# Optimization experiments

Measured on AMD Instinct MI355X. Metric: run time of the kernel, lower is better.

## Reference

```python
import jax, jax.numpy as jnp
import numpy as np

B, D, H, W_ = 2, 256, 64, 64


def setup_inputs() -> dict:
    key = jax.random.key(0)
    k1, k2 = jax.random.split(key)
    x = jax.random.normal(k1, (B, D, H, W_), dtype=jnp.float32)
    W = jax.random.normal(k2, (3 * D, D), dtype=jnp.float32) * 0.02  # 1x1 conv weight [out,in]
    b = jnp.zeros((3 * D,), dtype=jnp.float32)
    return {"x": x, "W": W, "b": b}


def reference(x, W, b):
    Bs, d, h, w = x.shape
    N = h * w
    sqrtV = d ** 0.25  # sqrt(sqrt(d)); q,k each divided -> qk^T / sqrt(d)
    # 1x1 conv == per-pixel linear over channels
    qkv = jnp.einsum('bchw,oc->bohw', x, W) + b[None, :, None, None]
    q, k, v = jnp.split(qkv, 3, axis=1)
    q = q.reshape(Bs, d, N).transpose(0, 2, 1) / sqrtV  # [B,N,d]
    k = k.reshape(Bs, d, N).transpose(0, 2, 1) / sqrtV
    v = v.reshape(Bs, d, N).transpose(0, 2, 1)
    # Sinkhorn (eps=1, max_iter=1, uniform marginals 1/N), log domain.
    # cost C = -q k^T  =>  -C = q k^T (softmax-style logits)
    negC = jnp.einsum('bnd,bmd->bnm', q, k)  # [B,N,N]
    logm = jnp.log(1.0 / N + 1e-8).astype(x.dtype)
    u = logm - jax.nn.logsumexp(negC, axis=-1)            # [B,N] row update
    vpot = logm - jax.nn.logsumexp(negC + u[..., None], axis=-2)  # [B,N] col update
    pi = jnp.exp(negC + u[..., None] + vpot[:, None, :])  # transport plan = attn
    out = jnp.einsum('bnm,bmd->bnd', pi, v)               # [B,N,d]
    return out.transpose(0, 2, 1).reshape(Bs, d, h, w)
```

## Files before the change

kernel.cpp:

```cpp
#include <hip/hip_runtime.h>
#include <hip/hip_bf16.h>
#include <math.h>

typedef __bf16 bf16;
typedef __bf16 bf16x8 __attribute__((ext_vector_type(8)));
typedef __bf16 bf16x4 __attribute__((ext_vector_type(4)));
typedef float floatx4 __attribute__((ext_vector_type(4)));

typedef const __attribute__((address_space(1))) void* gas_t;
typedef __attribute__((address_space(3))) void* las_t;

#define NPIX 4096
#define DCH 256

#define OFF_XB   ((size_t)0)
#define OFF_WB   ((size_t)4194304)
#define OFF_Q    ((size_t)4587520)
#define OFF_K    ((size_t)8781824)
#define OFF_V    ((size_t)12976128)
#define OFF_E    ((size_t)17170432)
#define OFF_VPP  ((size_t)84279296)
#define OFF_RP   ((size_t)88473600)
#define OFF_CP   ((size_t)89522176)
#define OFF_PART ((size_t)90570752)

__device__ __forceinline__ void stage_tile(const bf16* __restrict__ g0, size_t rstride,
                                           bf16* lds, int t) {
  const int wbase = (t >> 6) << 6;
#pragma unroll
  for (int i = 0; i < 4; i++) {
    int slot = i * 256 + t;
    int row = slot >> 3, seg = slot & 7;
    const bf16* g = g0 + (size_t)row * rstride + ((seg ^ (row & 7)) << 3);
    bf16* l = lds + (size_t)(i * 256 + wbase) * 8;
    __builtin_amdgcn_global_load_lds((gas_t)g, (las_t)l, 16, 0, 0);
  }
}

__device__ __forceinline__ void stage_tile512(const bf16* __restrict__ g0, size_t rstride,
                                              bf16* lds, int t) {
  const int wbase = (t >> 6) << 6;
#pragma unroll
  for (int i = 0; i < 4; i++) {
    int slot = i * 512 + t;
    int row = slot >> 3, seg = slot & 7;
    const bf16* g = g0 + (size_t)row * rstride + ((seg ^ (row & 7)) << 3);
    bf16* l = lds + (size_t)(i * 512 + wbase) * 8;
    __builtin_amdgcn_global_load_lds((gas_t)g, (las_t)l, 16, 0, 0);
  }
}

__device__ __forceinline__ void stage_tile128_512(const bf16* __restrict__ g0, size_t rstride,
                                                  bf16* lds, int t) {
  const int wbase = (t >> 6) << 6;
#pragma unroll
  for (int i = 0; i < 2; i++) {
    int slot = i * 512 + t;
    int row = slot >> 3, seg = slot & 7;
    const bf16* g = g0 + (size_t)row * rstride + ((seg ^ (row & 7)) << 3);
    bf16* l = lds + (size_t)(i * 512 + wbase) * 8;
    __builtin_amdgcn_global_load_lds((gas_t)g, (las_t)l, 16, 0, 0);
  }
}

__global__ __launch_bounds__(256) void prep(
    const float* __restrict__ x, const float* __restrict__ W,
    bf16* __restrict__ xb, bf16* __restrict__ wb)
{
  const int t = threadIdx.x;
  if (blockIdx.y == 4) {
    int gid = (blockIdx.z * 64 + blockIdx.x) * 256 + t;
    for (int i = gid; i < 49152; i += 32768) {
      float4 v = *(const float4*)(W + (size_t)i * 4);
      bf16x4 pk = { (bf16)v.x, (bf16)v.y, (bf16)v.z, (bf16)v.w };
      *(bf16x4*)(wb + (size_t)i * 4) = pk;
    }
    return;
  }
  __shared__ float ts[64][65];
  const int b = blockIdx.z, n0 = blockIdx.x * 64, c0 = blockIdx.y * 64;
  const float* xp = x + ((size_t)b * DCH + c0) * NPIX + n0;
  for (int i = 0; i < 4; i++) {
    int slot = t + i * 256;
    int c = slot >> 4, nq = (slot & 15) * 4;
    float4 v = *(const float4*)(xp + (size_t)c * NPIX + nq);
    ts[c][nq + 0] = v.x; ts[c][nq + 1] = v.y; ts[c][nq + 2] = v.z; ts[c][nq + 3] = v.w;
  }
  __syncthreads();
  for (int i = 0; i < 2; i++) {
    int slot = t + i * 256;
    int n = slot >> 3, cq = (slot & 7) * 8;
    bf16x8 pk;
    for (int j = 0; j < 8; j++) pk[j] = (bf16)ts[cq + j][n];
    *(bf16x8*)(xb + ((size_t)b * NPIX + n0 + n) * DCH + c0 + cq) = pk;
  }
}

__global__ __launch_bounds__(256) void conv_mfma(
    const bf16* __restrict__ xb, const bf16* __restrict__ wb,
    const float* __restrict__ bias,
    bf16* __restrict__ qb, bf16* __restrict__ kb, bf16* __restrict__ vb)
{
  __shared__ bf16 at[2][128 * 64];
  __shared__ bf16 bt[2][128 * 64];
  __shared__ float bs[128];
  const int t  = threadIdx.x;
  const int n0 = blockIdx.x * 128;
  const int o0 = blockIdx.y * 128;
  if (t < 128) bs[t] = bias[o0 + t];
  const int lane = t & 63, wave = t >> 6;
  const int wm = wave >> 1, wn = wave & 1;
  const int l15 = lane & 15, quad = lane >> 4;
  const int l7 = l15 & 7;

  stage_tile(wb + (size_t)o0 * DCH, DCH, at[0], t);
  stage_tile(xb + (size_t)n0 * DCH, DCH, bt[0], t);

  floatx4 acc[4][4];
  for (int i=0;i<4;i++) for (int j=0;j<4;j++) for (int r=0;r<4;r++) acc[i][j][r] = 0.f;

#pragma unroll
  for (int kidx = 0; kidx < 4; kidx++) {
    const int cur = kidx & 1;
    if (kidx < 3) {
      stage_tile(wb + (size_t)o0 * DCH + (kidx + 1) * 64, DCH, at[cur ^ 1], t);
      stage_tile(xb + (size_t)n0 * DCH + (kidx + 1) * 64, DCH, bt[cur ^ 1], t);
      asm volatile("s_waitcnt vmcnt(8)" ::: "memory");
    } else {
      asm volatile("s_waitcnt vmcnt(0)" ::: "memory");
    }
    __builtin_amdgcn_s_barrier();
    asm volatile("" ::: "memory");
    for (int kk = 0; kk < 2; kk++) {
      bf16x8 af[4], bfr[4];
      int sw = ((kk * 4 + quad) ^ l7) * 8;
      for (int f = 0; f < 4; f++)
        af[f]  = *(const bf16x8*)&at[cur][(wm*64 + f*16 + l15)*64 + sw];
      for (int f = 0; f < 4; f++)
        bfr[f] = *(const bf16x8*)&bt[cur][(wn*64 + f*16 + l15)*64 + sw];
      for (int fm = 0; fm < 4; fm++)
        for (int fn = 0; fn < 4; fn++)
          acc[fm][fn] = __builtin_amdgcn_mfma_f32_16x16x32_bf16(af[fm], bfr[fn], acc[fm][fn], 0, 0, 0);
    }
    asm volatile("" ::: "memory");
    __builtin_amdgcn_s_barrier();
  }

  const float scale = (o0 < 512) ? 0.25f : 1.0f;
  bf16* dst; int od;
  if (o0 < 256)      { dst = qb; od = o0; }
  else if (o0 < 512) { dst = kb; od = o0 - 256; }
  else               { dst = vb; od = o0 - 512; }

  for (int fm = 0; fm < 4; fm++)
    for (int fn = 0; fn < 4; fn++) {
      int o_l = wm*64 + fm*16 + quad*4;
      int n_g = n0 + wn*64 + fn*16 + l15;
      bf16x4 pk;
      for (int r = 0; r < 4; r++)
        pk[r] = (bf16)((acc[fm][fn][r] + bs[o_l + r]) * scale);
      *(bf16x4*)(dst + (size_t)n_g * DCH + od + o_l) = pk;
    }
}

__global__ __launch_bounds__(512, 2) void pass_a(
    const bf16* __restrict__ qb, const bf16* __restrict__ kb,
    bf16* __restrict__ E, float* __restrict__ rowpartG)
{
  __shared__ bf16 smem[65536];
  int flat = (int)blockIdx.x + ((int)blockIdx.y << 4) + ((int)blockIdx.z << 8);
  flat = (flat & 7) * 64 + (flat >> 3);
  const int bx = flat & 15, by = (flat >> 4) & 15, b = flat >> 8;
  qb += (size_t)b * NPIX * DCH;
  kb += (size_t)b * NPIX * DCH;
  E  += (size_t)b * NPIX * NPIX;
  float* rp = rowpartG + ((size_t)b * 16 + bx) * NPIX;
  const int t  = threadIdx.x;
  const int m0 = bx * 256;
  const int n0 = by * 256;
  const int lane = t & 63, wave = t >> 6;
  const int wm = wave >> 2, wn = wave & 3;
  const int l15 = lane & 15, quad = lane >> 4;
  const int l7 = l15 & 7;
  bf16* kt0 = smem;
  bf16* qt0 = smem + 32768;

  stage_tile512(kb + (size_t)m0 * DCH, DCH, kt0, t);
  stage_tile512(qb + (size_t)n0 * DCH, DCH, qt0, t);

  floatx4 acc[8][4];
  for (int i=0;i<8;i++) for (int j=0;j<4;j++) for (int r=0;r<4;r++) acc[i][j][r] = 0.f;

#pragma unroll
  for (int kidx = 0; kidx < 4; kidx++) {
    const int cur = kidx & 1;
    if (kidx < 3) {
      stage_tile512(kb + (size_t)m0 * DCH + (kidx + 1) * 64, DCH, kt0 + (cur ^ 1) * 16384, t);
      stage_tile512(qb + (size_t)n0 * DCH + (kidx + 1) * 64, DCH, qt0 + (cur ^ 1) * 16384, t);
      asm volatile("s_waitcnt vmcnt(8)" ::: "memory");
    } else {
      asm volatile("s_waitcnt vmcnt(0)" ::: "memory");
    }
    __builtin_amdgcn_s_barrier();
    asm volatile("" ::: "memory");
    for (int kk = 0; kk < 2; kk++) {
      bf16x8 af[8], bfr[4];
      int sw = ((kk * 4 + quad) ^ l7) * 8;
      for (int f = 0; f < 8; f++)
        af[f]  = *(const bf16x8*)&kt0[cur*16384 + (wm*128 + f*16 + l15)*64 + sw];
      for (int f = 0; f < 4; f++)
        bfr[f] = *(const bf16x8*)&qt0[cur*16384 + (wn*64 + f*16 + l15)*64 + sw];
      for (int fm = 0; fm < 8; fm++)
        for (int fn = 0; fn < 4; fn++)
          acc[fm][fn] = __builtin_amdgcn_mfma_f32_16x16x32_bf16(af[fm], bfr[fn], acc[fm][fn], 0, 0, 0);
    }
    asm volatile("" ::: "memory");
    __builtin_amdgcn_s_barrier();
  }

  bf16* ep = smem;
  for (int fm = 0; fm < 8; fm++)
    for (int fn = 0; fn < 4; fn++) {
      int n_loc = wn*64 + fn*16 + l15;
      int mby  = (wm*128 + fm*16 + quad*4) * 2;
      int addr = n_loc * 512 + mby;
      addr ^= (n_loc & 7) << 4;
      bf16x4 pk;
      for (int r = 0; r < 4; r++) pk[r] = (bf16)__expf(acc[fm][fn][r]);
      *(bf16x4*)((char*)ep + addr) = pk;
    }
  __syncthreads();
#pragma unroll
  for (int i = 0; i < 16; i++) {
    int slot = i * 512 + t;
    int nr = slot >> 5, c = slot & 31;
    int addr = nr * 512 + c * 16;
    addr ^= (nr & 7) << 4;
    bf16x8 v = *(const bf16x8*)((char*)ep + addr);
    *(bf16x8*)(E + (size_t)(n0 + nr) * NPIX + m0 + c * 8) = v;
    float s = 0.f;
    for (int j = 0; j < 8; j++) s += (float)v[j];
    s += __shfl_xor(s, 1); s += __shfl_xor(s, 2); s += __shfl_xor(s, 4);
    s += __shfl_xor(s, 8); s += __shfl_xor(s, 16);
    if ((t & 31) == 0) rp[n0 + nr] = s;
  }
}

__global__ __launch_bounds__(256) void col_pass(
    const bf16* __restrict__ E, const float* __restrict__ rowpartG,
    float* __restrict__ colpartG, float logm)
{
  __shared__ float eus[128];
  const int b = blockIdx.z;
  E += (size_t)b * NPIX * NPIX;
  const float* rp = rowpartG + (size_t)b * 16 * NPIX;
  float* cp = colpartG + ((size_t)b * 32 + blockIdx.y) * NPIX;
  const int t = threadIdx.x;
  const int col = blockIdx.x * 1024 + t * 4;
  const int nbase = blockIdx.y * 128;
  if (t < 128) {
    float s = 0.f;
    for (int mi = 0; mi < 16; mi++) s += rp[(size_t)mi * NPIX + nbase + t];
    eus[t] = __expf(logm - __logf(s));
  }
  __syncthreads();
  float a0 = 0.f, a1 = 0.f, a2 = 0.f, a3 = 0.f;
  for (int r = 0; r < 128; r++) {
    float eu = eus[r];
    bf16x4 ev = *(const bf16x4*)(E + (size_t)(nbase + r) * NPIX + col);
    a0 += eu * (float)ev[0];
    a1 += eu * (float)ev[1];
    a2 += eu * (float)ev[2];
    a3 += eu * (float)ev[3];
  }
  float4 o = {a0, a1, a2, a3};
  *(float4*)(cp + col) = o;
}

__global__ __launch_bounds__(256) void vpp_kernel(
    const bf16* __restrict__ vb, const float* __restrict__ colpartG,
    bf16* __restrict__ vppT, float logm)
{
  __shared__ float ts[64][65];
  __shared__ float ef[64];
  const int b = blockIdx.z;
  vb += (size_t)b * NPIX * DCH;
  const float* cp = colpartG + (size_t)b * 32 * NPIX;
  vppT += (size_t)b * DCH * NPIX;
  const int t = threadIdx.x;
  const int m0 = blockIdx.x * 64, d0 = blockIdx.y * 64;
  if (t < 64) {
    float s = 0.f;
    for (int g = 0; g < 32; g++) s += cp[(size_t)g * NPIX + m0 + t];
    ef[t] = __expf(logm - __logf(s));
  }
  __syncthreads();
  for (int i = 0; i < 2; i++) {
    int slot = t + i * 256;
    int m = slot >> 3, dq = (slot & 7) * 8;
    bf16x8 v = *(const bf16x8*)(vb + (size_t)(m0 + m) * DCH + d0 + dq);
    float s = ef[m];
    for (int j = 0; j < 8; j++) ts[dq + j][m] = s * (float)v[j];
  }
  __syncthreads();
  for (int i = 0; i < 2; i++) {
    int slot = t + i * 256;
    int d = slot >> 3, mq = (slot & 7) * 8;
    bf16x8 pk;
    for (int j = 0; j < 8; j++) pk[j] = (bf16)ts[d][mq + j];
    *(bf16x8*)(vppT + (size_t)(d0 + d) * NPIX + m0 + mq) = pk;
  }
}

__global__ __launch_bounds__(512, 2) void pass_c(
    const bf16* __restrict__ E, const bf16* __restrict__ vppT,
    const float* __restrict__ rowpartG, bf16* __restrict__ part, float logm)
{
  __shared__ bf16 smem[49152];
  __shared__ float eus[128];
  const int z = blockIdx.z;
  const int b = z >> 2, kc = z & 3;
  E += (size_t)b * NPIX * NPIX;
  vppT += (size_t)b * DCH * NPIX;
  const float* rpg = rowpartG + (size_t)b * 16 * NPIX;
  part += (size_t)(b * 4 + kc) * DCH * NPIX;
  const int t  = threadIdx.x;
  const int n0 = blockIdx.x * 128;
  const int mstart = kc * 1024;
  if (t < 128) {
    float s = 0.f;
    for (int mi = 0; mi < 16; mi++) s += rpg[(size_t)mi * NPIX + n0 + t];
    eus[t] = __expf(logm - __logf(s));
  }
  const int lane = t & 63, wave = t >> 6;
  const int wn = wave >> 2, wd = wave & 3;
  const int l15 = lane & 15, quad = lane >> 4;
  const int l7 = l15 & 7;
  bf16* et0 = smem;
  bf16* vt0 = smem + 16384;

  floatx4 acc[4][4];
  for (int i=0;i<4;i++) for (int j=0;j<4;j++) for (int r=0;r<4;r++) acc[i][j][r] = 0.f;
  __syncthreads();

  stage_tile128_512(E + (size_t)n0 * NPIX + mstart, NPIX, et0, t);
  stage_tile512(vppT + mstart, NPIX, vt0, t);

#pragma unroll 4
  for (int kidx = 0; kidx < 16; kidx++) {
    const int cur = kidx & 1;
    if (kidx < 15) {
      const int kn = mstart + (kidx + 1) * 64;
      stage_tile128_512(E + (size_t)n0 * NPIX + kn, NPIX, et0 + (cur ^ 1) * 8192, t);
      stage_tile512(vppT + kn, NPIX, vt0 + (cur ^ 1) * 16384, t);
      asm volatile("s_waitcnt vmcnt(6)" ::: "memory");
    } else {
      asm volatile("s_waitcnt vmcnt(0)" ::: "memory");
    }
    __builtin_amdgcn_s_barrier();
    asm volatile("" ::: "memory");
    for (int kk = 0; kk < 2; kk++) {
      bf16x8 af[4], bfr[4];
      int sw = ((kk * 4 + quad) ^ l7) * 8;
      for (int f = 0; f < 4; f++)
        af[f]  = *(const bf16x8*)&et0[cur*8192  + (wn*64 + f*16 + l15)*64 + sw];
      for (int f = 0; f < 4; f++)
        bfr[f] = *(const bf16x8*)&vt0[cur*16384 + (wd*64 + f*16 + l15)*64 + sw];
      for (int fn = 0; fn < 4; fn++)
        for (int fd = 0; fd < 4; fd++)
          acc[fn][fd] = __builtin_amdgcn_mfma_f32_16x16x32_bf16(af[fn], bfr[fd], acc[fn][fd], 0, 0, 0);
    }
    asm volatile("" ::: "memory");
    __builtin_amdgcn_s_barrier();
  }

  bf16* ept = smem;
  for (int fn = 0; fn < 4; fn++)
    for (int fd = 0; fd < 4; fd++) {
      int d_loc = wd*64 + fd*16 + l15;
      int n_l   = wn*64 + fn*16 + quad*4;
      int addr = d_loc * 256 + n_l * 2;
      addr ^= (d_loc & 7) << 4;
      bf16x4 o;
      for (int r = 0; r < 4; r++) o[r] = (bf16)(acc[fn][fd][r] * eus[n_l + r]);
      *(bf16x4*)((char*)ept + addr) = o;
    }
  __syncthreads();
#pragma unroll
  for (int i = 0; i < 8; i++) {
    int slot = i * 512 + t;
    int dr = slot >> 4, c = slot & 15;
    int addr = dr * 256 + c * 16;
    addr ^= (dr & 7) << 4;
    bf16x8 v = *(const bf16x8*)((char*)ept + addr);
    *(bf16x8*)(part + (size_t)dr * NPIX + n0 + c * 8) = v;
  }
}

__global__ __launch_bounds__(256) void reduce_k(
    const bf16* __restrict__ part, float* __restrict__ outp)
{
  size_t i4 = ((size_t)blockIdx.x * 256 + threadIdx.x) * 4;
  size_t b = i4 >> 20;
  size_t off = i4 & (size_t)1048575;
  const bf16* p = part + b * 4 * (size_t)1048576 + off;
  bf16x4 a = *(const bf16x4*)(p);
  bf16x4 bq = *(const bf16x4*)(p + (size_t)1048576);
  bf16x4 c = *(const bf16x4*)(p + (size_t)2097152);
  bf16x4 d = *(const bf16x4*)(p + (size_t)3145728);
  float4 s = { (float)a[0]+(float)bq[0]+(float)c[0]+(float)d[0],
               (float)a[1]+(float)bq[1]+(float)c[1]+(float)d[1],
               (float)a[2]+(float)bq[2]+(float)c[2]+(float)d[2],
               (float)a[3]+(float)bq[3]+(float)c[3]+(float)d[3] };
  *(float4*)(outp + i4) = s;
}

extern "C" void kernel_launch(void* const* d_in, const int* in_sizes, int n_in,
                              void* d_out, int out_size, void* d_ws, size_t ws_size,
                              hipStream_t stream) {
  (void)in_sizes; (void)n_in; (void)out_size; (void)ws_size;
  const float* x    = (const float*)d_in[0];
  const float* Wm   = (const float*)d_in[1];
  const float* bias = (const float*)d_in[2];
  float* outp = (float*)d_out;
  char* ws = (char*)d_ws;

  bf16*  xb   = (bf16*)(ws + OFF_XB);
  bf16*  wb   = (bf16*)(ws + OFF_WB);
  bf16*  qb   = (bf16*)(ws + OFF_Q);
  bf16*  kb   = (bf16*)(ws + OFF_K);
  bf16*  vb   = (bf16*)(ws + OFF_V);
  bf16*  E    = (bf16*)(ws + OFF_E);
  bf16*  vppT = (bf16*)(ws + OFF_VPP);
  float* rp   = (float*)(ws + OFF_RP);
  float* cp   = (float*)(ws + OFF_CP);
  bf16*  part = (bf16*)(ws + OFF_PART);

  const float logm = logf(1.0f / 4096.0f + 1e-8f);

  prep<<<dim3(64, 5, 2), 256, 0, stream>>>(x, Wm, xb, wb);
  conv_mfma<<<dim3(64, 6), 256, 0, stream>>>(xb, wb, bias, qb, kb, vb);

  pass_a<<<dim3(16, 16, 2), 512, 0, stream>>>(qb, kb, E, rp);
  col_pass<<<dim3(4, 32, 2), 256, 0, stream>>>(E, rp, cp, logm);
  vpp_kernel<<<dim3(64, 4, 2), 256, 0, stream>>>(vb, cp, vppT, logm);
  pass_c<<<dim3(32, 1, 8), 512, 0, stream>>>(E, vppT, rp, part, logm);
  reduce_k<<<2048, 256, 0, stream>>>(part, outp);
}
```

Baseline: 152.6 us.

## Retile pass_c to 256-row tiles with 8-way split-K and XCD-aware block remap

pass_c now computes a 256(n)x256(d) output tile per block instead of 128x256, doubling A-fragment reuse of each staged vppT tile. The K range is split 8 ways instead of 4, keeping the grid at 256 blocks, and a flat block-index remap groups blocks across XCDs. reduce_k is extended to sum 8 bf16 partials, and col_pass's inner loop gets an unroll pragma. In exchange, partial-sum traffic doubles, and LDS use grows to about 128KB, which likely limits occupancy to one block per CU despite the launch bound.

```diff
diff --git a/kernel.cpp b/kernel.cpp
--- a/kernel.cpp
+++ b/kernel.cpp
@@ -42,19 +42,6 @@
   const int wbase = (t >> 6) << 6;
 #pragma unroll
   for (int i = 0; i < 4; i++) {
-    int slot = i * 512 + t;
-    int row = slot >> 3, seg = slot & 7;
-    const bf16* g = g0 + (size_t)row * rstride + ((seg ^ (row & 7)) << 3);
-    bf16* l = lds + (size_t)(i * 512 + wbase) * 8;
-    __builtin_amdgcn_global_load_lds((gas_t)g, (las_t)l, 16, 0, 0);
-  }
-}
-
-__device__ __forceinline__ void stage_tile128_512(const bf16* __restrict__ g0, size_t rstride,
-                                                  bf16* lds, int t) {
-  const int wbase = (t >> 6) << 6;
-#pragma unroll
-  for (int i = 0; i < 2; i++) {
     int slot = i * 512 + t;
     int row = slot >> 3, seg = slot & 7;
     const bf16* g = g0 + (size_t)row * rstride + ((seg ^ (row & 7)) << 3);
@@ -265,6 +252,7 @@
   }
   __syncthreads();
   float a0 = 0.f, a1 = 0.f, a2 = 0.f, a3 = 0.f;
+#pragma unroll 4
   for (int r = 0; r < 128; r++) {
     float eu = eus[r];
     bf16x4 ev = *(const bf16x4*)(E + (size_t)(nbase + r) * NPIX + col);
@@ -316,18 +304,20 @@
     const bf16* __restrict__ E, const bf16* __restrict__ vppT,
     const float* __restrict__ rowpartG, bf16* __restrict__ part, float logm)
 {
-  __shared__ bf16 smem[49152];
-  __shared__ float eus[128];
-  const int z = blockIdx.z;
-  const int b = z >> 2, kc = z & 3;
+  __shared__ bf16 smem[65536];
+  __shared__ float eus[256];
+  int flat = (int)blockIdx.x + ((int)blockIdx.z << 4);
+  flat = (flat & 7) * 32 + (flat >> 3);
+  const int nx = flat & 15, zz = flat >> 4;
+  const int b = zz >> 3, kc = zz & 7;
   E += (size_t)b * NPIX * NPIX;
   vppT += (size_t)b * DCH * NPIX;
   const float* rpg = rowpartG + (size_t)b * 16 * NPIX;
-  part += (size_t)(b * 4 + kc) * DCH * NPIX;
+  part += (size_t)(b * 8 + kc) * DCH * NPIX;
   const int t  = threadIdx.x;
-  const int n0 = blockIdx.x * 128;
-  const int mstart = kc * 1024;
-  if (t < 128) {
+  const int n0 = nx * 256;
+  const int mstart = kc * 512;
+  if (t < 256) {
     float s = 0.f;
     for (int mi = 0; mi < 16; mi++) s += rpg[(size_t)mi * NPIX + n0 + t];
     eus[t] = __expf(logm - __logf(s));
@@ -337,60 +327,60 @@
   const int l15 = lane & 15, quad = lane >> 4;
   const int l7 = l15 & 7;
   bf16* et0 = smem;
-  bf16* vt0 = smem + 16384;
-
-  floatx4 acc[4][4];
-  for (int i=0;i<4;i++) for (int j=0;j<4;j++) for (int r=0;r<4;r++) acc[i][j][r] = 0.f;
-  __syncthreads();
-
-  stage_tile128_512(E + (size_t)n0 * NPIX + mstart, NPIX, et0, t);
+  bf16* vt0 = smem + 32768;
+
+  floatx4 acc[8][4];
+  for (int i=0;i<8;i++) for (int j=0;j<4;j++) for (int r=0;r<4;r++) acc[i][j][r] = 0.f;
+  __syncthreads();
+
+  stage_tile512(E + (size_t)n0 * NPIX + mstart, NPIX, et0, t);
   stage_tile512(vppT + mstart, NPIX, vt0, t);
 
-#pragma unroll 4
-  for (int kidx = 0; kidx < 16; kidx++) {
+#pragma unroll
+  for (int kidx = 0; kidx < 8; kidx++) {
     const int cur = kidx & 1;
-    if (kidx < 15) {
+    if (kidx < 7) {
       const int kn = mstart + (kidx + 1) * 64;
-      stage_tile128_512(E + (size_t)n0 * NPIX + kn, NPIX, et0 + (cur ^ 1) * 8192, t);
+      stage_tile512(E + (size_t)n0 * NPIX + kn, NPIX, et0 + (cur ^ 1) * 16384, t);
       stage_tile512(vppT + kn, NPIX, vt0 + (cur ^ 1) * 16384, t);
-      asm volatile("s_waitcnt vmcnt(6)" ::: "memory");
+      asm volatile("s_waitcnt vmcnt(8)" ::: "memory");
     } else {
       asm volatile("s_waitcnt vmcnt(0)" ::: "memory");
     }
     __builtin_amdgcn_s_barrier();
     asm volatile("" ::: "memory");
     for (int kk = 0; kk < 2; kk++) {
-      bf16x8 af[4], bfr[4];
+      bf16x8 af[8], bfr[4];
       int sw = ((kk * 4 + quad) ^ l7) * 8;
-      for (int f = 0; f < 4; f++)
-        af[f]  = *(const bf16x8*)&et0[cur*8192  + (wn*64 + f*16 + l15)*64 + sw];
+      for (int f = 0; f < 8; f++)
+        af[f]  = *(const bf16x8*)&et0[cur*16384 + (wn*128 + f*16 + l15)*64 + sw];
       for (int f = 0; f < 4; f++)
         bfr[f] = *(const bf16x8*)&vt0[cur*16384 + (wd*64 + f*16 + l15)*64 + sw];
-      for (int fn = 0; fn < 4; fn++)
-        for (int fd = 0; fd < 4; fd++)
-          acc[fn][fd] = __builtin_amdgcn_mfma_f32_16x16x32_bf16(af[fn], bfr[fd], acc[fn][fd], 0, 0, 0);
+      for (int fm = 0; fm < 8; fm++)
+        for (int fn = 0; fn < 4; fn++)
+          acc[fm][fn] = __builtin_amdgcn_mfma_f32_16x16x32_bf16(af[fm], bfr[fn], acc[fm][fn], 0, 0, 0);
     }
     asm volatile("" ::: "memory");
     __builtin_amdgcn_s_barrier();
   }
 
   bf16* ept = smem;
-  for (int fn = 0; fn < 4; fn++)
-    for (int fd = 0; fd < 4; fd++) {
-      int d_loc = wd*64 + fd*16 + l15;
-      int n_l   = wn*64 + fn*16 + quad*4;
-      int addr = d_loc * 256 + n_l * 2;
+  for (int fm = 0; fm < 8; fm++)
+    for (int fn = 0; fn < 4; fn++) {
+      int d_loc = wd*64 + fn*16 + l15;
+      int n_l   = wn*128 + fm*16 + quad*4;
+      int addr = d_loc * 512 + n_l * 2;
       addr ^= (d_loc & 7) << 4;
       bf16x4 o;
-      for (int r = 0; r < 4; r++) o[r] = (bf16)(acc[fn][fd][r] * eus[n_l + r]);
+      for (int r = 0; r < 4; r++) o[r] = (bf16)(acc[fm][fn][r] * eus[n_l + r]);
       *(bf16x4*)((char*)ept + addr) = o;
     }
   __syncthreads();
 #pragma unroll
-  for (int i = 0; i < 8; i++) {
+  for (int i = 0; i < 16; i++) {
     int slot = i * 512 + t;
-    int dr = slot >> 4, c = slot & 15;
-    int addr = dr * 256 + c * 16;
+    int dr = slot >> 5, c = slot & 31;
+    int addr = dr * 512 + c * 16;
     addr ^= (dr & 7) << 4;
     bf16x8 v = *(const bf16x8*)((char*)ept + addr);
     *(bf16x8*)(part + (size_t)dr * NPIX + n0 + c * 8) = v;
@@ -403,15 +393,13 @@
   size_t i4 = ((size_t)blockIdx.x * 256 + threadIdx.x) * 4;
   size_t b = i4 >> 20;
   size_t off = i4 & (size_t)1048575;
-  const bf16* p = part + b * 4 * (size_t)1048576 + off;
-  bf16x4 a = *(const bf16x4*)(p);
-  bf16x4 bq = *(const bf16x4*)(p + (size_t)1048576);
-  bf16x4 c = *(const bf16x4*)(p + (size_t)2097152);
-  bf16x4 d = *(const bf16x4*)(p + (size_t)3145728);
-  float4 s = { (float)a[0]+(float)bq[0]+(float)c[0]+(float)d[0],
-               (float)a[1]+(float)bq[1]+(float)c[1]+(float)d[1],
-               (float)a[2]+(float)bq[2]+(float)c[2]+(float)d[2],
-               (float)a[3]+(float)bq[3]+(float)c[3]+(float)d[3] };
+  const bf16* p = part + b * 8 * (size_t)1048576 + off;
+  float4 s = {0.f, 0.f, 0.f, 0.f};
+#pragma unroll
+  for (int j = 0; j < 8; j++) {
+    bf16x4 v = *(const bf16x4*)(p + (size_t)j * 1048576);
+    s.x += (float)v[0]; s.y += (float)v[1]; s.z += (float)v[2]; s.w += (float)v[3];
+  }
   *(float4*)(outp + i4) = s;
 }
 
@@ -444,6 +432,6 @@
   pass_a<<<dim3(16, 16, 2), 512, 0, stream>>>(qb, kb, E, rp);
   col_pass<<<dim3(4, 32, 2), 256, 0, stream>>>(E, rp, cp, logm);
   vpp_kernel<<<dim3(64, 4, 2), 256, 0, stream>>>(vb, cp, vppT, logm);
-  pass_c<<<dim3(32, 1, 8), 512, 0, stream>>>(E, vppT, rp, part, logm);
+  pass_c<<<dim3(16, 1, 16), 512, 0, stream>>>(E, vppT, rp, part, logm);
   reduce_k<<<2048, 256, 0, stream>>>(part, outp);
 }
```

After: 156.5 us. 2.6% more time.
